# Optimization experiments

Hardware: AMD Instinct MI355X
Metric: run time of the kernel (lower is better)

The kernel has to match this reference:

```python
import jax, jax.numpy as jnp
import numpy as np

BS, D, C, S = 256, 1024, 262144, 32768  # batch, layer_size, num_class, num_c_layers (cr*num_class)


def setup_inputs() -> dict:
    key = jax.random.key(0)
    k_x, k_w, k_b, k_ids, k_san, k_t = jax.random.split(key, 6)
    x = jax.random.normal(k_x, (BS, D), dtype=jnp.float32)
    # nn.Linear weight init: uniform(-0.05, 0.05); bias trained, so give it small values
    weight = jax.random.uniform(k_w, (C, D), dtype=jnp.float32, minval=-0.05, maxval=0.05)
    bias = jax.random.uniform(k_b, (C,), dtype=jnp.float32, minval=-0.01, maxval=0.01)
    # gan: global active neuron ids selected by LSH (size num_c_layers)
    sample_ids = jnp.sort(jax.random.randint(k_ids, (S,), 0, C))
    # san: per-sample active-neuron mask within the sampled set
    san = jax.random.uniform(k_san, (BS, S)) < 0.5
    # new_targets: label restricted to active set, normalized by per-row nonzeros
    targets = jax.random.uniform(k_t, (BS, S), dtype=jnp.float32) * san.astype(jnp.float32)
    targets = targets / jnp.sum(targets, axis=1, keepdims=True)
    return {"x": x, "weight": weight, "bias": bias, "targets": targets,
            "sample_ids": sample_ids, "san": san}


def reference(x, weight, bias, targets, sample_ids, san):
    # gather sampled class weights / biases (F.embedding + indexed bias)
    sample_w = weight[sample_ids]           # [S, D]
    sample_b = bias[sample_ids]             # [S]
    # logits over sampled classes
    logits = jnp.einsum('bd,sd->bs', x, sample_w) + sample_b  # [BS, S]
    # mask inactive neurons per sample with float32 min (as in torch code)
    neg = jnp.finfo(jnp.float32).min
    logits = jnp.where(san, logits, neg)
    log_sm = jax.nn.log_softmax(logits, axis=1) * san.astype(logits.dtype)
    # masked soft cross-entropy loss
    return -jnp.mean(jnp.sum(log_sm * targets, axis=1))
```

## Files before the change

### kernel.cpp

```cpp
#include <hip/hip_runtime.h>
#include <stdint.h>

#define BSZ 256
#define DIM 1024
#define NS  32768
#define BN  64
#define BK  64
#define NBLK (NS / BN)

typedef __attribute__((ext_vector_type(8))) short bf16x8;
typedef __attribute__((ext_vector_type(4))) float f32x4;
typedef __attribute__((ext_vector_type(8))) unsigned short u16x8;

__device__ __forceinline__ unsigned short f2b(float f) {
    union { float f; uint32_t u; } v; v.f = f;
    uint32_t u = v.u;
    return (unsigned short)((u + 0x7fffu + ((u >> 16) & 1u)) >> 16);
}

__global__ __launch_bounds__(256)
void k_cvt_x(const float4* __restrict__ x, ushort4* __restrict__ xb) {
    int i = blockIdx.x * 256 + threadIdx.x;
    float4 v = x[i];
    ushort4 o;
    o.x = f2b(v.x); o.y = f2b(v.y); o.z = f2b(v.z); o.w = f2b(v.w);
    xb[i] = o;
}

__global__ __launch_bounds__(256)
void k_gemm(const unsigned short* __restrict__ xb,
            const float* __restrict__ weight,
            const float* __restrict__ bias,
            const int* __restrict__ sids,
            const float* __restrict__ targets,
            float* __restrict__ partials)
{
    __shared__ __align__(16) unsigned short Ald[BSZ * BK];
    __shared__ __align__(16) unsigned short Bld[BN * BK];

    const int t    = threadIdx.x;
    const int w    = t >> 6;
    const int lane = t & 63;
    const int n0   = blockIdx.x * BN;

    int aoff[8];
#pragma unroll
    for (int i = 0; i < 8; ++i) {
        int flat = i * 256 + t;
        int m  = flat >> 3;
        int cc = (flat & 7) ^ (m & 7);
        aoff[i] = m * DIM + cc * 8;
    }

    const int na = t >> 3;
    const int ca = t & 7;
    const float* wp0 = weight + (size_t)sids[n0 + na] * DIM + ca * 8;
    const float* wp1 = weight + (size_t)sids[n0 + na + 32] * DIM + ca * 8;
    unsigned short* bd0 = &Bld[na * BK + ((ca ^ (na & 7)) * 8)];
    const int nb = na + 32;
    unsigned short* bd1 = &Bld[nb * BK + ((ca ^ (nb & 7)) * 8)];

    f32x4 acc[4][4];
#pragma unroll
    for (int i = 0; i < 4; ++i)
#pragma unroll
        for (int j = 0; j < 4; ++j) acc[i][j] = (f32x4)0.0f;

    float4 v0 = *(const float4*)(wp0 + 0);
    float4 v1 = *(const float4*)(wp0 + 4);
    float4 v2 = *(const float4*)(wp1 + 0);
    float4 v3 = *(const float4*)(wp1 + 4);

    for (int kk = 0; kk < DIM; kk += BK) {
        __syncthreads();
#pragma unroll
        for (int i = 0; i < 8; ++i) {
            const unsigned short* g = xb + aoff[i] + kk;
            unsigned short* l = &Ald[(i * 256 + (w << 6)) * 8];
            __builtin_amdgcn_global_load_lds(
                (const __attribute__((address_space(1))) void*)g,
                (__attribute__((address_space(3))) void*)l, 16, 0, 0);
        }
        {
            u16x8 p;
            p[0]=f2b(v0.x); p[1]=f2b(v0.y); p[2]=f2b(v0.z); p[3]=f2b(v0.w);
            p[4]=f2b(v1.x); p[5]=f2b(v1.y); p[6]=f2b(v1.z); p[7]=f2b(v1.w);
            *(u16x8*)bd0 = p;
            u16x8 q;
            q[0]=f2b(v2.x); q[1]=f2b(v2.y); q[2]=f2b(v2.z); q[3]=f2b(v2.w);
            q[4]=f2b(v3.x); q[5]=f2b(v3.y); q[6]=f2b(v3.z); q[7]=f2b(v3.w);
            *(u16x8*)bd1 = q;
        }
        __syncthreads();

        if (kk + BK < DIM) {
            v0 = *(const float4*)(wp0 + kk + BK);
            v1 = *(const float4*)(wp0 + kk + BK + 4);
            v2 = *(const float4*)(wp1 + kk + BK);
            v3 = *(const float4*)(wp1 + kk + BK + 4);
        }

        const int qd = lane >> 4;
        const int r  = lane & 15;
#pragma unroll
        for (int ks = 0; ks < 2; ++ks) {
            bf16x8 av[4], bv[4];
#pragma unroll
            for (int mt = 0; mt < 4; ++mt) {
                int m  = (w << 6) + mt * 16 + r;
                int cc = (ks * 4 + qd) ^ (m & 7);
                av[mt] = *(const bf16x8*)&Ald[m * BK + cc * 8];
            }
#pragma unroll
            for (int nt = 0; nt < 4; ++nt) {
                int n  = nt * 16 + r;
                int cc = (ks * 4 + qd) ^ (n & 7);
                bv[nt] = *(const bf16x8*)&Bld[n * BK + cc * 8];
            }
#pragma unroll
            for (int mt = 0; mt < 4; ++mt)
#pragma unroll
                for (int nt = 0; nt < 4; ++nt)
                    acc[mt][nt] = __builtin_amdgcn_mfma_f32_16x16x32_bf16(
                        av[mt], bv[nt], acc[mt][nt], 0, 0, 0);
        }
    }

    const int qd = lane >> 4;
    const int r  = lane & 15;
    float bv_[4];
#pragma unroll
    for (int nt = 0; nt < 4; ++nt) bv_[nt] = bias[sids[n0 + nt * 16 + r]];

#pragma unroll
    for (int mt = 0; mt < 4; ++mt) {
#pragma unroll
        for (int j = 0; j < 4; ++j) {
            const int row = (w << 6) + mt * 16 + qd * 4 + j;
            const float* tp = targets + (size_t)row * NS + n0 + r;
            float l[4], tg[4];
#pragma unroll
            for (int nt = 0; nt < 4; ++nt) {
                l[nt]  = acc[mt][nt][j] + bv_[nt];
                tg[nt] = tp[nt * 16];
            }
            float m = -1e30f;
#pragma unroll
            for (int nt = 0; nt < 4; ++nt)
                if (tg[nt] > 0.f) m = fmaxf(m, l[nt]);
#pragma unroll
            for (int off = 8; off > 0; off >>= 1)
                m = fmaxf(m, __shfl_xor(m, off));
            float s = 0.f, tl = 0.f, ts = 0.f;
#pragma unroll
            for (int nt = 0; nt < 4; ++nt) {
                if (tg[nt] > 0.f) {
                    s  += __expf(l[nt] - m);
                    tl  = fmaf(tg[nt], l[nt], tl);
                    ts += tg[nt];
                }
            }
#pragma unroll
            for (int off = 8; off > 0; off >>= 1) {
                s  += __shfl_xor(s, off);
                tl += __shfl_xor(tl, off);
                ts += __shfl_xor(ts, off);
            }
            if (r == 0) {
                float4 o = {m, s, tl, ts};
                *(float4*)(partials + (((size_t)row * NBLK) + blockIdx.x) * 4) = o;
            }
        }
    }
}

__global__ __launch_bounds__(256)
void k_merge(const float4* __restrict__ partials, float* __restrict__ rowloss) {
    const int row = blockIdx.x;
    const int t   = threadIdx.x;
    const float4* p = partials + (size_t)row * NBLK;
    float4 a = p[t];
    float4 b = p[t + 256];
    float m  = fmaxf(a.x, b.x);
    float s  = a.y * __expf(a.x - m) + b.y * __expf(b.x - m);
    float tl = a.z + b.z;
    float ts = a.w + b.w;
#pragma unroll
    for (int off = 32; off > 0; off >>= 1) {
        float m2 = __shfl_xor(m, off);
        float s2 = __shfl_xor(s, off);
        float nm = fmaxf(m, m2);
        s = s * __expf(m - nm) + s2 * __expf(m2 - nm);
        m = nm;
        tl += __shfl_xor(tl, off);
        ts += __shfl_xor(ts, off);
    }
    __shared__ float sm[4], ss[4], stl[4], sts[4];
    if ((t & 63) == 0) { int w = t >> 6; sm[w] = m; ss[w] = s; stl[w] = tl; sts[w] = ts; }
    __syncthreads();
    if (t == 0) {
        float M = fmaxf(fmaxf(sm[0], sm[1]), fmaxf(sm[2], sm[3]));
        float S = 0.f, TL = 0.f, TS = 0.f;
        for (int i = 0; i < 4; ++i) { S += ss[i] * __expf(sm[i] - M); TL += stl[i]; TS += sts[i]; }
        rowloss[row] = TL - TS * (M + logf(S));
    }
}

__global__ __launch_bounds__(256)
void k_final(const float* __restrict__ rowloss, float* __restrict__ out) {
    int t = threadIdx.x;
    float v = rowloss[t];
#pragma unroll
    for (int off = 32; off > 0; off >>= 1) v += __shfl_xor(v, off);
    __shared__ float p[4];
    if ((t & 63) == 0) p[t >> 6] = v;
    __syncthreads();
    if (t == 0) out[0] = -(p[0] + p[1] + p[2] + p[3]) / 256.0f;
}

extern "C" void kernel_launch(void* const* d_in, const int* in_sizes, int n_in,
                              void* d_out, int out_size, void* d_ws, size_t ws_size,
                              hipStream_t stream) {
    const float* x       = (const float*)d_in[0];
    const float* weight  = (const float*)d_in[1];
    const float* bias    = (const float*)d_in[2];
    const float* targets = (const float*)d_in[3];
    const int*   sids    = (const int*)d_in[4];
    float* out = (float*)d_out;

    char* ws = (char*)d_ws;
    unsigned short* xb = (unsigned short*)ws;
    float* partials = (float*)(ws + (1 << 20));
    float* rowloss  = (float*)(ws + (1 << 20) + (2 << 20));

    k_cvt_x <<<(BSZ * DIM / 4) / 256, 256, 0, stream>>>((const float4*)x, (ushort4*)xb);
    k_gemm  <<<NS / BN, 256, 0, stream>>>(xb, weight, bias, sids, targets, partials);
    k_merge <<<BSZ, 256, 0, stream>>>((const float4*)partials, rowloss);
    k_final <<<1, 256, 0, stream>>>(rowloss, out);
}
```

Measured before the change: 1.220 ms.

## Double-buffer LDS tiles to overlap staging with MFMA compute

```diff
diff --git a/kernel.cpp b/kernel.cpp
--- a/kernel.cpp
+++ b/kernel.cpp
@@ -35,8 +35,10 @@
             const float* __restrict__ targets,
             float* __restrict__ partials)
 {
-    __shared__ __align__(16) unsigned short Ald[BSZ * BK];
-    __shared__ __align__(16) unsigned short Bld[BN * BK];
+    __shared__ __align__(16) unsigned short Ald0[BSZ * BK];
+    __shared__ __align__(16) unsigned short Ald1[BSZ * BK];
+    __shared__ __align__(16) unsigned short Bld0[BN * BK];
+    __shared__ __align__(16) unsigned short Bld1[BN * BK];
 
     const int t    = threadIdx.x;
     const int w    = t >> 6;
@@ -56,9 +58,9 @@
     const int ca = t & 7;
     const float* wp0 = weight + (size_t)sids[n0 + na] * DIM + ca * 8;
     const float* wp1 = weight + (size_t)sids[n0 + na + 32] * DIM + ca * 8;
-    unsigned short* bd0 = &Bld[na * BK + ((ca ^ (na & 7)) * 8)];
     const int nb = na + 32;
-    unsigned short* bd1 = &Bld[nb * BK + ((ca ^ (nb & 7)) * 8)];
+    const int bd0off = na * BK + ((ca ^ (na & 7)) * 8);
+    const int bd1off = nb * BK + ((ca ^ (nb & 7)) * 8);
 
     f32x4 acc[4][4];
 #pragma unroll
@@ -66,42 +68,23 @@
 #pragma unroll
         for (int j = 0; j < 4; ++j) acc[i][j] = (f32x4)0.0f;
 
-    float4 v0 = *(const float4*)(wp0 + 0);
-    float4 v1 = *(const float4*)(wp0 + 4);
-    float4 v2 = *(const float4*)(wp1 + 0);
-    float4 v3 = *(const float4*)(wp1 + 4);
-
-    for (int kk = 0; kk < DIM; kk += BK) {
-        __syncthreads();
+    float4 e0, e1, e2, e3;
+    float4 o0, o1, o2, o3;
+
+    const int qd = lane >> 4;
+    const int r  = lane & 15;
+
+    auto stageA = [&](unsigned short* Abuf, int kk) {
 #pragma unroll
         for (int i = 0; i < 8; ++i) {
             const unsigned short* g = xb + aoff[i] + kk;
-            unsigned short* l = &Ald[(i * 256 + (w << 6)) * 8];
+            unsigned short* l = &Abuf[(i * 256 + (w << 6)) * 8];
             __builtin_amdgcn_global_load_lds(
                 (const __attribute__((address_space(1))) void*)g,
                 (__attribute__((address_space(3))) void*)l, 16, 0, 0);
         }
-        {
-            u16x8 p;
-            p[0]=f2b(v0.x); p[1]=f2b(v0.y); p[2]=f2b(v0.z); p[3]=f2b(v0.w);
-            p[4]=f2b(v1.x); p[5]=f2b(v1.y); p[6]=f2b(v1.z); p[7]=f2b(v1.w);
-            *(u16x8*)bd0 = p;
-            u16x8 q;
-            q[0]=f2b(v2.x); q[1]=f2b(v2.y); q[2]=f2b(v2.z); q[3]=f2b(v2.w);
-            q[4]=f2b(v3.x); q[5]=f2b(v3.y); q[6]=f2b(v3.z); q[7]=f2b(v3.w);
-            *(u16x8*)bd1 = q;
-        }
-        __syncthreads();
-
-        if (kk + BK < DIM) {
-            v0 = *(const float4*)(wp0 + kk + BK);
-            v1 = *(const float4*)(wp0 + kk + BK + 4);
-            v2 = *(const float4*)(wp1 + kk + BK);
-            v3 = *(const float4*)(wp1 + kk + BK + 4);
-        }
-
-        const int qd = lane >> 4;
-        const int r  = lane & 15;
+    };
+    auto compute = [&](const unsigned short* Abuf, const unsigned short* Bbuf) {
 #pragma unroll
         for (int ks = 0; ks < 2; ++ks) {
             bf16x8 av[4], bv[4];
@@ -109,25 +92,69 @@
             for (int mt = 0; mt < 4; ++mt) {
                 int m  = (w << 6) + mt * 16 + r;
                 int cc = (ks * 4 + qd) ^ (m & 7);
-                av[mt] = *(const bf16x8*)&Ald[m * BK + cc * 8];
+                av[mt] = *(const bf16x8*)&Abuf[m * BK + cc * 8];
             }
 #pragma unroll
             for (int nt = 0; nt < 4; ++nt) {
                 int n  = nt * 16 + r;
                 int cc = (ks * 4 + qd) ^ (n & 7);
-                bv[nt] = *(const bf16x8*)&Bld[n * BK + cc * 8];
-            }
+                bv[nt] = *(const bf16x8*)&Bbuf[n * BK + cc * 8];
+            }
+            __builtin_amdgcn_s_setprio(1);
 #pragma unroll
             for (int mt = 0; mt < 4; ++mt)
 #pragma unroll
                 for (int nt = 0; nt < 4; ++nt)
                     acc[mt][nt] = __builtin_amdgcn_mfma_f32_16x16x32_bf16(
                         av[mt], bv[nt], acc[mt][nt], 0, 0, 0);
-        }
-    }
-
-    const int qd = lane >> 4;
-    const int r  = lane & 15;
+            __builtin_amdgcn_s_setprio(0);
+        }
+    };
+    auto packStore = [&](unsigned short* Bbuf,
+                         const float4& a, const float4& b,
+                         const float4& c, const float4& d) {
+        u16x8 p;
+        p[0]=f2b(a.x); p[1]=f2b(a.y); p[2]=f2b(a.z); p[3]=f2b(a.w);
+        p[4]=f2b(b.x); p[5]=f2b(b.y); p[6]=f2b(b.z); p[7]=f2b(b.w);
+        *(u16x8*)&Bbuf[bd0off] = p;
+        u16x8 q;
+        q[0]=f2b(c.x); q[1]=f2b(c.y); q[2]=f2b(c.z); q[3]=f2b(c.w);
+        q[4]=f2b(d.x); q[5]=f2b(d.y); q[6]=f2b(d.z); q[7]=f2b(d.w);
+        *(u16x8*)&Bbuf[bd1off] = q;
+    };
+
+    stageA(Ald0, 0);
+    e0 = *(const float4*)(wp0);     e1 = *(const float4*)(wp0 + 4);
+    e2 = *(const float4*)(wp1);     e3 = *(const float4*)(wp1 + 4);
+    packStore(Bld0, e0, e1, e2, e3);
+    e0 = *(const float4*)(wp0 + BK);     e1 = *(const float4*)(wp0 + BK + 4);
+    e2 = *(const float4*)(wp1 + BK);     e3 = *(const float4*)(wp1 + BK + 4);
+    __syncthreads();
+
+    for (int kk = 0; kk < DIM; kk += 2 * BK) {
+        if (kk + BK < DIM) stageA(Ald1, kk + BK);
+        if (kk + 2 * BK < DIM) {
+            o0 = *(const float4*)(wp0 + kk + 2 * BK);
+            o1 = *(const float4*)(wp0 + kk + 2 * BK + 4);
+            o2 = *(const float4*)(wp1 + kk + 2 * BK);
+            o3 = *(const float4*)(wp1 + kk + 2 * BK + 4);
+        }
+        compute(Ald0, Bld0);
+        if (kk + BK < DIM) packStore(Bld1, e0, e1, e2, e3);
+        __syncthreads();
+
+        if (kk + 2 * BK < DIM) stageA(Ald0, kk + 2 * BK);
+        if (kk + 3 * BK < DIM) {
+            e0 = *(const float4*)(wp0 + kk + 3 * BK);
+            e1 = *(const float4*)(wp0 + kk + 3 * BK + 4);
+            e2 = *(const float4*)(wp1 + kk + 3 * BK);
+            e3 = *(const float4*)(wp1 + kk + 3 * BK + 4);
+        }
+        if (kk + BK < DIM) compute(Ald1, Bld1);
+        if (kk + 2 * BK < DIM) packStore(Bld0, o0, o1, o2, o3);
+        __syncthreads();
+    }
+
     float bv_[4];
 #pragma unroll
     for (int nt = 0; nt < 4; ++nt) bv_[nt] = bias[sids[n0 + nt * 16 + r]];
```

New measurement: 1.201 ms. Within noise of the previous version (-1.6%).
